# Kernel tuning notes

Hardware: AMD Instinct MI355X
Metric: run time of the kernel (lower is better)

Reference implementation:

```python
import jax, jax.numpy as jnp
import numpy as np

D = 512
EPS = 1e-5  # torch BatchNorm1d default eps


def swish(x):
    return x * jax.nn.sigmoid(x)


def batchnorm_train(x, gamma, beta):
    # BatchNorm1d in training mode: biased batch stats
    m = jnp.mean(x, axis=0)
    v = jnp.mean((x - m) ** 2, axis=0)
    return gamma * (x - m) / jnp.sqrt(v + EPS) + beta


def setup_inputs() -> dict:
    key = jax.random.key(0)
    k_fea, k_w1, k_w2, k_lerp = jax.random.split(key, 4)
    bs, P = 32768, 8192
    fea = jax.random.normal(k_fea, (bs, D), dtype=jnp.float32)
    # first P rows are the minority (positive) class
    lbl = jnp.concatenate([jnp.ones((P, 1), jnp.int32), jnp.zeros((bs - P, 1), jnp.int32)], axis=0)
    scale = 1.0 / np.sqrt(D)
    W1 = jax.random.normal(k_w1, (D, D), dtype=jnp.float32) * scale
    W2 = jax.random.normal(k_w2, (D, D), dtype=jnp.float32) * scale
    b1 = jnp.zeros((D,), jnp.float32)
    b2 = jnp.zeros((D,), jnp.float32)
    g1 = jnp.ones((D,), jnp.float32)
    g2 = jnp.ones((D,), jnp.float32)
    beta1 = jnp.zeros((D,), jnp.float32)
    beta2 = jnp.zeros((D,), jnp.float32)
    lerp_w = jax.random.uniform(k_lerp, (P, 3), dtype=jnp.float32)
    return dict(fea=fea, lbl=lbl, W1=W1, b1=b1, g1=g1, beta1=beta1,
                W2=W2, b2=b2, g2=g2, beta2=beta2, lerp_w=lerp_w, num_pos=P)


def reference(fea, lbl, W1, b1, g1, beta1, W2, b2, g2, beta2, lerp_w, num_pos):
    # fea_transform: Linear -> BN -> Swish -> Linear -> BN -> Swish
    h = swish(batchnorm_train(fea @ W1 + b1, g1, beta1))
    h = swish(batchnorm_train(h @ W2 + b2, g2, beta2))

    # SMOTE path (training mode): KNN over positive-class features
    pos_idx = jnp.nonzero(lbl[:, 0] > 0, size=num_pos)[0]  # static-size gather
    x = h[pos_idx]                                          # (P, D)
    sq = jnp.sum(x * x, axis=-1)                            # (P,)
    # negative squared pairwise distance; topk largest == nearest
    neg_dist = 2.0 * (x @ x.T) - sq[:, None] - sq[None, :]  # (P, P)
    _, idx = jax.lax.top_k(neg_dist, 3)                     # (P, 3), idx[:,0] == self

    a = x[idx[:, 0]]                                        # (P, D) anchor
    b = x[idx]                                              # (P, 3, D) neighbors
    # torch.lerp(a, b, w) = a + w * (b - a), one random w per (i, j)
    new_fea = a[:, None, :] + lerp_w[..., None] * (b - a[:, None, :])
    new_fea = new_fea.reshape(-1, D)                        # (3P, D), row-major matches i,j loop order

    fea_out = jnp.concatenate([h, new_fea], axis=0)
    lbl_out = jnp.concatenate([lbl, jnp.ones((new_fea.shape[0], 1), lbl.dtype)], axis=0)
    return fea_out, lbl_out
```

## Files before the change

kernel.cpp:

```cpp
#include <hip/hip_runtime.h>
#include <math.h>

#define NEG_INF -3.402823466e38f
#define NSPLIT 8

typedef __attribute__((ext_vector_type(8))) short bf16x8;
typedef __attribute__((ext_vector_type(4))) float f32x4;

__device__ __forceinline__ void gload_lds16(const unsigned short* g, unsigned short* l) {
  __builtin_amdgcn_global_load_lds(
      (const __attribute__((address_space(1))) unsigned int*)g,
      (__attribute__((address_space(3))) unsigned int*)l, 16, 0, 0);
}
__device__ __forceinline__ void gload_lds16f(const float* g, float* l) {
  __builtin_amdgcn_global_load_lds(
      (const __attribute__((address_space(1))) unsigned int*)g,
      (__attribute__((address_space(3))) unsigned int*)l, 16, 0, 0);
}

__device__ __forceinline__ unsigned short f2bf(float f) {
  union { float f; unsigned int u; } a; a.f = f;
  unsigned int u = a.u;
  return (unsigned short)((u + 0x7fffu + ((u >> 16) & 1u)) >> 16);
}

__device__ __forceinline__ void split3_8(f32x4 a, f32x4 b,
                                         bf16x8& hi, bf16x8& md, bf16x8& lo) {
  union { bf16x8 v; unsigned int u[4]; } H, M, L;
  float f[8];
  f[0]=a[0]; f[1]=a[1]; f[2]=a[2]; f[3]=a[3];
  f[4]=b[0]; f[5]=b[1]; f[6]=b[2]; f[7]=b[3];
#pragma unroll
  for (int p = 0; p < 4; ++p) {
    union { float f; unsigned int u; } x0, x1, h0, h1, r0, r1, m0, m1, s0, s1;
    x0.f = f[2*p]; x1.f = f[2*p+1];
    H.u[p] = (x0.u >> 16) | (x1.u & 0xffff0000u);
    h0.u = x0.u & 0xffff0000u; h1.u = x1.u & 0xffff0000u;
    r0.f = x0.f - h0.f;        r1.f = x1.f - h1.f;
    M.u[p] = (r0.u >> 16) | (r1.u & 0xffff0000u);
    m0.u = r0.u & 0xffff0000u; m1.u = r1.u & 0xffff0000u;
    s0.f = r0.f - m0.f;        s1.f = r1.f - m1.f;
    L.u[p] = (s0.u >> 16) | (s1.u & 0xffff0000u);
  }
  hi = H.v; md = M.v; lo = L.v;
}

__global__ __launch_bounds__(256) void split_w_t3(const float* __restrict__ W,
    unsigned short* __restrict__ Th, unsigned short* __restrict__ Tm,
    unsigned short* __restrict__ Tl)
{
  __shared__ float T[64][65];
  int k0 = blockIdx.x * 64, n0 = blockIdx.y * 64;
  int tid = threadIdx.x;
  int r = tid >> 4, c4 = (tid & 15) << 2;
#pragma unroll
  for (int p = 0; p < 4; ++p) {
    int row = r + p * 16;
    float4 v = *(const float4*)&W[(size_t)(k0 + row) * 512 + n0 + c4];
    T[c4 + 0][row] = v.x; T[c4 + 1][row] = v.y;
    T[c4 + 2][row] = v.z; T[c4 + 3][row] = v.w;
  }
  __syncthreads();
  int nr = tid >> 2, kc = (tid & 3) << 4;
#pragma unroll
  for (int u = 0; u < 16; ++u) {
    union { float f; unsigned int u; } x, h, rr, m, ss;
    x.f = T[nr][kc + u];
    unsigned short hb = (unsigned short)(x.u >> 16);
    h.u = x.u & 0xffff0000u;
    rr.f = x.f - h.f;
    unsigned short mb = (unsigned short)(rr.u >> 16);
    m.u = rr.u & 0xffff0000u;
    ss.f = rr.f - m.f;
    unsigned short lb = (unsigned short)(ss.u >> 16);
    size_t o = (size_t)(n0 + nr) * 512 + k0 + kc + u;
    Th[o] = hb; Tm[o] = mb; Tl[o] = lb;
  }
}

__global__ __launch_bounds__(256, 2) void gemm_split3(
    const float* __restrict__ A, const unsigned short* __restrict__ Bth,
    const unsigned short* __restrict__ Btm, const unsigned short* __restrict__ Btl,
    const float* __restrict__ bias, float* __restrict__ C, float* __restrict__ partial)
{
  __shared__ float sA[128 * 64];
  __shared__ unsigned short sBh[128 * 64];
  __shared__ unsigned short sBm[128 * 64];
  __shared__ unsigned short sBl[128 * 64];
  const int tid = threadIdx.x;
  const int w = tid >> 6, lane = tid & 63;
  const int wr = w >> 1, wc = w & 1;
  const int bm = blockIdx.x * 128, bn = blockIdx.y * 128;
  const int fr = lane & 15, fg = lane >> 4;
  const int arow = tid >> 4, acb = (tid & 15) << 4;
  const int brow = tid >> 3, bcb = (tid & 7) << 4;

  f32x4 acc[4][4];
#pragma unroll
  for (int mi = 0; mi < 4; ++mi)
#pragma unroll
    for (int ni = 0; ni < 4; ++ni) acc[mi][ni] = (f32x4){0.f, 0.f, 0.f, 0.f};

  for (int kt = 0; kt < 512; kt += 64) {
#pragma unroll
    for (int p = 0; p < 8; ++p) {
      int row = arow + p * 16;
      int swz = ((row & 3) << 5) | ((row & 4) << 2);
      int cb = acb ^ swz;
      gload_lds16f(&A[(size_t)(bm + row) * 512 + kt + (cb >> 2)],
                   &sA[row * 64 + (acb >> 2)]);
    }
#pragma unroll
    for (int p = 0; p < 4; ++p) {
      int row = brow + p * 32;
      int cb = bcb ^ ((row & 7) << 4);
      int so = (bcb >> 1);
      gload_lds16(&Bth[(size_t)(bn + row) * 512 + kt + (cb >> 1)], &sBh[row * 64 + so]);
      gload_lds16(&Btm[(size_t)(bn + row) * 512 + kt + (cb >> 1)], &sBm[row * 64 + so]);
      gload_lds16(&Btl[(size_t)(bn + row) * 512 + kt + (cb >> 1)], &sBl[row * 64 + so]);
    }
    __syncthreads();
#pragma unroll
    for (int ks = 0; ks < 2; ++ks) {
      int kbb = ks * 64 + fg * 16;
      bf16x8 bfh[4], bfm[4], bfl[4];
#pragma unroll
      for (int ni = 0; ni < 4; ++ni) {
        int row = wc * 64 + ni * 16 + fr;
        int off = row * 64 + ((kbb ^ ((row & 7) << 4)) >> 1);
        bfh[ni] = *(const bf16x8*)&sBh[off];
        bfm[ni] = *(const bf16x8*)&sBm[off];
        bfl[ni] = *(const bf16x8*)&sBl[off];
      }
      bf16x8 afh[4], afm[4], afl[4];
      int kba = ks * 128 + fg * 32;
#pragma unroll
      for (int mi = 0; mi < 4; ++mi) {
        int row = wr * 64 + mi * 16 + fr;
        int swz = ((row & 3) << 5) | ((row & 4) << 2);
        f32x4 f0 = *(const f32x4*)((const char*)sA + row * 256 + (kba ^ swz));
        f32x4 f1 = *(const f32x4*)((const char*)sA + row * 256 + ((kba + 16) ^ swz));
        split3_8(f0, f1, afh[mi], afm[mi], afl[mi]);
      }
#pragma unroll
      for (int mi = 0; mi < 4; ++mi)
#pragma unroll
        for (int ni = 0; ni < 4; ++ni) {
          acc[mi][ni] = __builtin_amdgcn_mfma_f32_16x16x32_bf16(afl[mi], bfh[ni], acc[mi][ni], 0, 0, 0);
          acc[mi][ni] = __builtin_amdgcn_mfma_f32_16x16x32_bf16(afm[mi], bfm[ni], acc[mi][ni], 0, 0, 0);
          acc[mi][ni] = __builtin_amdgcn_mfma_f32_16x16x32_bf16(afh[mi], bfl[ni], acc[mi][ni], 0, 0, 0);
          acc[mi][ni] = __builtin_amdgcn_mfma_f32_16x16x32_bf16(afm[mi], bfh[ni], acc[mi][ni], 0, 0, 0);
          acc[mi][ni] = __builtin_amdgcn_mfma_f32_16x16x32_bf16(afh[mi], bfm[ni], acc[mi][ni], 0, 0, 0);
          acc[mi][ni] = __builtin_amdgcn_mfma_f32_16x16x32_bf16(afh[mi], bfh[ni], acc[mi][ni], 0, 0, 0);
        }
    }
    __syncthreads();
  }
  float bno[4], s[4] = {0, 0, 0, 0}, q[4] = {0, 0, 0, 0};
#pragma unroll
  for (int ni = 0; ni < 4; ++ni) bno[ni] = bias[bn + wc * 64 + ni * 16 + fr];
#pragma unroll
  for (int mi = 0; mi < 4; ++mi) {
    int row = bm + wr * 64 + mi * 16 + fg * 4;
#pragma unroll
    for (int ni = 0; ni < 4; ++ni) {
      int col = bn + wc * 64 + ni * 16 + fr;
#pragma unroll
      for (int r = 0; r < 4; ++r) {
        float v = acc[mi][ni][r] + bno[ni];
        C[(size_t)(row + r) * 512 + col] = v;
        s[ni] += v; q[ni] += v * v;
      }
    }
  }
#pragma unroll
  for (int ni = 0; ni < 4; ++ni) {
    float ss = s[ni], qq = q[ni];
    ss += __shfl_xor(ss, 16); ss += __shfl_xor(ss, 32);
    qq += __shfl_xor(qq, 16); qq += __shfl_xor(qq, 32);
    if (fg == 0) {
      int slot = blockIdx.x * 2 + wr;
      int col = bn + wc * 64 + ni * 16 + fr;
      partial[(size_t)(slot * 2 + 0) * 512 + col] = ss;
      partial[(size_t)(slot * 2 + 1) * 512 + col] = qq;
    }
  }
}

__global__ __launch_bounds__(256) void bn_reduce1(
    const float* __restrict__ partial, float* __restrict__ partial2, int nslot)
{
  int g = blockIdx.x, p = blockIdx.y;
  int per = nslot >> 4;
  int t = threadIdx.x;
#pragma unroll
  for (int cc = 0; cc < 2; ++cc) {
    int c = t + cc * 256;
    float s = 0.f;
    for (int s0 = 0; s0 < per; ++s0) {
      int slot = g * per + s0;
      s += partial[(size_t)(slot * 2 + p) * 512 + c];
    }
    partial2[(size_t)(g * 2 + p) * 512 + c] = s;
  }
}

__global__ void bn_finalize(
    const float* __restrict__ partial2, const float* __restrict__ g,
    const float* __restrict__ beta, float* __restrict__ scale,
    float* __restrict__ shift, int rows)
{
  int c = blockIdx.x * blockDim.x + threadIdx.x;
  if (c >= 512) return;
  float s = 0, s2 = 0;
  for (int b = 0; b < 16; ++b) {
    s  += partial2[(size_t)(b * 2 + 0) * 512 + c];
    s2 += partial2[(size_t)(b * 2 + 1) * 512 + c];
  }
  float m = s / rows;
  float v = s2 / rows - m * m;
  if (v < 0) v = 0;
  float sc = g[c] / sqrtf(v + 1e-5f);
  scale[c] = sc;
  shift[c] = beta[c] - m * sc;
}

__global__ void bn_swish(
    const float* __restrict__ Y, const float* __restrict__ scale,
    const float* __restrict__ shift, float* __restrict__ H, int total4)
{
  int i = blockIdx.x * blockDim.x + threadIdx.x;
  if (i >= total4) return;
  float4 y = ((const float4*)Y)[i];
  int c = (i * 4) & 511;
  float z;
  float4 o;
  z = y.x * scale[c + 0] + shift[c + 0]; o.x = z / (1.f + expf(-z));
  z = y.y * scale[c + 1] + shift[c + 1]; o.y = z / (1.f + expf(-z));
  z = y.z * scale[c + 2] + shift[c + 2]; o.z = z / (1.f + expf(-z));
  z = y.w * scale[c + 3] + shift[c + 3]; o.w = z / (1.f + expf(-z));
  ((float4*)H)[i] = o;
}

__global__ void compact_pos(const int* __restrict__ lbl, int n,
                            int* __restrict__ pos, int P)
{
  __shared__ int base;
  __shared__ int wsum[16];
  int tid = threadIdx.x;
  int nthr = blockDim.x;
  for (int t = tid; t < P; t += nthr) pos[t] = 0;
  if (tid == 0) base = 0;
  __syncthreads();
  int nw = nthr >> 6;
  for (int start = 0; start < n; start += nthr) {
    int i = start + tid;
    int pred = (i < n) && (lbl[i] > 0);
    unsigned long long m = __ballot(pred);
    int wid = tid >> 6, lane = tid & 63;
    if (lane == 0) wsum[wid] = __popcll(m);
    __syncthreads();
    int wbase = 0;
    for (int w2 = 0; w2 < wid; ++w2) wbase += wsum[w2];
    int rank = base + wbase + __popcll(m & ((1ull << lane) - 1ull));
    if (pred && rank < P) pos[rank] = i;
    __syncthreads();
    if (tid == 0) { int t2 = 0; for (int w2 = 0; w2 < nw; ++w2) t2 += wsum[w2]; base += t2; }
    __syncthreads();
  }
}

__global__ void gather_sq(const float* __restrict__ H, const int* __restrict__ pos,
                          float* __restrict__ X, unsigned short* __restrict__ Xh,
                          float* __restrict__ sq)
{
  int r = blockIdx.x, t = threadIdx.x;
  int src = pos[r];
  float4 v = *(const float4*)&H[src * 512 + t * 4];
  *(float4*)&X[r * 512 + t * 4] = v;
  ushort4 hv;
  hv.x = f2bf(v.x); hv.y = f2bf(v.y); hv.z = f2bf(v.z); hv.w = f2bf(v.w);
  *(ushort4*)&Xh[r * 512 + t * 4] = hv;
  float s = v.x * v.x + v.y * v.y + v.z * v.z + v.w * v.w;
#pragma unroll
  for (int off = 32; off > 0; off >>= 1) s += __shfl_down(s, off);
  __shared__ float red[2];
  if ((t & 63) == 0) red[t >> 6] = s;
  __syncthreads();
  if (t == 0) sq[r] = red[0] + red[1];
}

__global__ __launch_bounds__(256, 2) void gram8(
    const unsigned short* __restrict__ Xh, const float* __restrict__ sq, int P,
    float* __restrict__ p8v, int* __restrict__ p8j)
{
  __shared__ unsigned short Ah[128 * 64];
  __shared__ unsigned short Bh[128 * 64];
  __shared__ float dl[4][64][17];
  __shared__ float sqj_l[128];

  const int tid = threadIdx.x;
  const int w = tid >> 6, lane = tid & 63;
  const int wr = w >> 1, wc = w & 1;
  const int bi = blockIdx.x * 128;
  const int jchunk = P / NSPLIT;
  const int jlo = blockIdx.y * jchunk;

  const int srow = tid >> 3;
  const int scb  = (tid & 7) << 4;
  const int fr = lane & 15, fg = lane >> 4;

  float t[8]; int ji[8];
#pragma unroll
  for (int q = 0; q < 8; ++q) { t[q] = NEG_INF; ji[q] = 0x7fffffff; }

  for (int jt = 0; jt < jchunk; jt += 128) {
    const int j0 = jlo + jt;
    if (tid < 128) sqj_l[tid] = sq[j0 + tid];
    f32x4 acc[4][4];
#pragma unroll
    for (int mi = 0; mi < 4; ++mi)
#pragma unroll
      for (int ni = 0; ni < 4; ++ni) acc[mi][ni] = (f32x4){0.f, 0.f, 0.f, 0.f};

    for (int kt = 0; kt < 512; kt += 64) {
#pragma unroll
      for (int it = 0; it < 4; ++it) {
        int row = srow + it * 32;
        int cb = scb ^ ((row & 7) << 4);
        gload_lds16(&Xh[(size_t)(bi + row) * 512 + kt + (cb >> 1)],
                    &Ah[row * 64 + (scb >> 1)]);
        gload_lds16(&Xh[(size_t)(j0 + row) * 512 + kt + (cb >> 1)],
                    &Bh[row * 64 + (scb >> 1)]);
      }
      __syncthreads();
#pragma unroll
      for (int ks = 0; ks < 2; ++ks) {
        bf16x8 af[4], bfr[4];
        int kb = ks * 64 + fg * 16;
#pragma unroll
        for (int mi = 0; mi < 4; ++mi) {
          int row = wr * 64 + mi * 16 + fr;
          af[mi] = *(const bf16x8*)&Ah[row * 64 + ((kb ^ ((row & 7) << 4)) >> 1)];
        }
#pragma unroll
        for (int ni = 0; ni < 4; ++ni) {
          int row = wc * 64 + ni * 16 + fr;
          bfr[ni] = *(const bf16x8*)&Bh[row * 64 + ((kb ^ ((row & 7) << 4)) >> 1)];
        }
#pragma unroll
        for (int mi = 0; mi < 4; ++mi)
#pragma unroll
          for (int ni = 0; ni < 4; ++ni)
            acc[mi][ni] = __builtin_amdgcn_mfma_f32_16x16x32_bf16(
                af[mi], bfr[ni], acc[mi][ni], 0, 0, 0);
      }
      __syncthreads();
    }

#pragma unroll
    for (int qn = 0; qn < 4; ++qn) {
      float sqv = sqj_l[wc * 64 + qn * 16 + fr];
#pragma unroll
      for (int mi = 0; mi < 4; ++mi)
#pragma unroll
        for (int r = 0; r < 4; ++r)
          dl[w][mi * 16 + fg * 4 + r][fr] = 2.0f * acc[mi][qn][r] - sqv;
      __syncthreads();
      int jbase = j0 + wc * 64 + qn * 16;
      for (int c = 0; c < 16; ++c) {
        float v = dl[w][lane][c];
        if (v > t[7]) {
          t[7] = v; ji[7] = jbase + c;
#pragma unroll
          for (int q = 7; q > 0; --q) {
            if (t[q] > t[q - 1]) {
              float tv = t[q]; t[q] = t[q - 1]; t[q - 1] = tv;
              int tj = ji[q]; ji[q] = ji[q - 1]; ji[q - 1] = tj;
            }
          }
        }
      }
      __syncthreads();
    }
  }

  int row = bi + wr * 64 + lane;
  int set = blockIdx.y * 2 + wc;
  size_t base = ((size_t)row * (NSPLIT * 2) + set) * 8;
#pragma unroll
  for (int q = 0; q < 8; ++q) { p8v[base + q] = t[q]; p8j[base + q] = ji[q]; }
}

__global__ void merge8(const float* __restrict__ p8v, const int* __restrict__ p8j,
                       int* __restrict__ cand, int P)
{
  int i = blockIdx.x * blockDim.x + threadIdx.x;
  if (i >= P) return;
  const int S = NSPLIT * 2;
  int head[S];
#pragma unroll
  for (int s = 0; s < S; ++s) head[s] = 0;
  const float* v = p8v + (size_t)i * S * 8;
  const int* j = p8j + (size_t)i * S * 8;
  for (int k = 0; k < 8; ++k) {
    float bv = NEG_INF; int bj = 0x7fffffff; int bs = 0;
#pragma unroll
    for (int s = 0; s < S; ++s) {
      if (head[s] < 8) {
        float vv = v[s * 8 + head[s]];
        int jj = j[s * 8 + head[s]];
        if (vv > bv || (vv == bv && jj < bj)) { bv = vv; bj = jj; bs = s; }
      }
    }
    head[bs]++;
    cand[i * 8 + k] = bj;
  }
}

__global__ __launch_bounds__(64) void rescore(
    const float* __restrict__ X, const float* __restrict__ sq,
    const int* __restrict__ cand, int* __restrict__ idx3)
{
  int i = blockIdx.x;
  int lane = threadIdx.x;
  f32x4 x0 = *(const f32x4*)&X[(size_t)i * 512 + lane * 8];
  f32x4 x1 = *(const f32x4*)&X[(size_t)i * 512 + lane * 8 + 4];
  float d[8]; int cj[8];
#pragma unroll
  for (int c = 0; c < 8; ++c) {
    int j = cand[i * 8 + c];
    cj[c] = j;
    f32x4 y0 = *(const f32x4*)&X[(size_t)j * 512 + lane * 8];
    f32x4 y1 = *(const f32x4*)&X[(size_t)j * 512 + lane * 8 + 4];
    float p = x0.x * y0.x + x0.y * y0.y + x0.z * y0.z + x0.w * y0.w
            + x1.x * y1.x + x1.y * y1.y + x1.z * y1.z + x1.w * y1.w;
#pragma unroll
    for (int off = 32; off > 0; off >>= 1) p += __shfl_xor(p, off);
    d[c] = 2.0f * p - sq[i] - sq[j];
  }
  if (lane == 0) {
    for (int k = 0; k < 3; ++k) {
      int b = 0;
#pragma unroll
      for (int c = 1; c < 8; ++c)
        if (d[c] > d[b] || (d[c] == d[b] && cj[c] < cj[b])) b = c;
      idx3[i * 3 + k] = cj[b];
      d[b] = NEG_INF; cj[b] = 0x7fffffff;
    }
  }
}

__global__ void make_newfea(const float* __restrict__ X, const int* __restrict__ idx3,
                            const float* __restrict__ lw, float* __restrict__ out)
{
  int r = blockIdx.x;
  int i = r / 3, k = r - i * 3;
  int ai = idx3[i * 3 + 0];
  int bi = idx3[i * 3 + k];
  float w = lw[r];
  int t = threadIdx.x;
  float4 av = *(const float4*)&X[ai * 512 + t * 4];
  float4 bv = *(const float4*)&X[bi * 512 + t * 4];
  float4 o;
  o.x = av.x + w * (bv.x - av.x);
  o.y = av.y + w * (bv.y - av.y);
  o.z = av.z + w * (bv.z - av.z);
  o.w = av.w + w * (bv.w - av.w);
  *(float4*)&out[(size_t)r * 512 + t * 4] = o;
}

__global__ void write_lbl(const int* __restrict__ lbl, float* __restrict__ out,
                          int n_in, int n_total)
{
  int i = blockIdx.x * blockDim.x + threadIdx.x;
  if (i < n_total) out[i] = (i < n_in) ? (float)lbl[i] : 1.0f;
}

extern "C" void kernel_launch(void* const* d_in, const int* in_sizes, int n_in,
                              void* d_out, int out_size, void* d_ws, size_t ws_size,
                              hipStream_t stream)
{
  const float* fea   = (const float*)d_in[0];
  const int*   lbl   = (const int*)d_in[1];
  const float* W1    = (const float*)d_in[2];
  const float* b1    = (const float*)d_in[3];
  const float* g1    = (const float*)d_in[4];
  const float* beta1 = (const float*)d_in[5];
  const float* W2    = (const float*)d_in[6];
  const float* b2    = (const float*)d_in[7];
  const float* g2    = (const float*)d_in[8];
  const float* beta2 = (const float*)d_in[9];
  const float* lerp_w = (const float*)d_in[10];

  int bs = in_sizes[0] / 512;
  int P  = in_sizes[10] / 3;
  int n_total = bs + 3 * P;

  float* out_f = (float*)d_out;
  float* Hout = out_f;
  float* newfea = out_f + (size_t)bs * 512;
  float* lbl_out = out_f + (size_t)n_total * 512;

  const size_t MB = 1024 * 1024;
  const size_t KB = 1024;
  char* ws = (char*)d_ws;
  float* Y1 = (float*)ws;
  float* X  = (float*)(ws + 64 * MB);
  unsigned short* W1h = (unsigned short*)(ws + 64 * MB);
  unsigned short* W1m = (unsigned short*)(ws + 64 * MB + 512 * KB);
  unsigned short* W1l = (unsigned short*)(ws + 64 * MB + 1024 * KB);
  unsigned short* W2h = (unsigned short*)(ws + 64 * MB + 1536 * KB);
  unsigned short* W2m = (unsigned short*)(ws + 64 * MB + 2048 * KB);
  unsigned short* W2l = (unsigned short*)(ws + 64 * MB + 2560 * KB);
  float* partial = (float*)(ws + 80 * MB);
  float* scale = (float*)(ws + 82 * MB);
  float* shiftv = scale + 512;
  float* sq = shiftv + 512;
  int* pos = (int*)(sq + 8192);
  int* idx3 = pos + 8192;
  float* partial2 = (float*)(ws + 83 * MB);
  unsigned short* Xh = (unsigned short*)ws;
  float* p8v = (float*)(ws + 8 * MB);
  int*   p8j = (int*)(ws + 12 * MB);
  int*   cand = (int*)(ws + 16 * MB);

  dim3 wgrid(8, 8);
  split_w_t3<<<wgrid, 256, 0, stream>>>(W1, W1h, W1m, W1l);
  split_w_t3<<<wgrid, 256, 0, stream>>>(W2, W2h, W2m, W2l);

  dim3 ggrid(bs / 128, 4);
  int nslot = (bs / 128) * 2;
  dim3 rgrid(16, 2);

  gemm_split3<<<ggrid, 256, 0, stream>>>(fea, W1h, W1m, W1l, b1, Y1, partial);
  bn_reduce1<<<rgrid, 256, 0, stream>>>(partial, partial2, nslot);
  bn_finalize<<<2, 256, 0, stream>>>(partial2, g1, beta1, scale, shiftv, bs);
  bn_swish<<<(bs * 512 / 4 + 255) / 256, 256, 0, stream>>>(Y1, scale, shiftv, Y1, bs * 512 / 4);

  gemm_split3<<<ggrid, 256, 0, stream>>>(Y1, W2h, W2m, W2l, b2, Hout, partial);
  bn_reduce1<<<rgrid, 256, 0, stream>>>(partial, partial2, nslot);
  bn_finalize<<<2, 256, 0, stream>>>(partial2, g2, beta2, scale, shiftv, bs);
  bn_swish<<<(bs * 512 / 4 + 255) / 256, 256, 0, stream>>>(Hout, scale, shiftv, Hout, bs * 512 / 4);

  compact_pos<<<1, 1024, 0, stream>>>(lbl, bs, pos, P);
  gather_sq<<<P, 128, 0, stream>>>(Hout, pos, X, Xh, sq);

  dim3 gram_grid(P / 128, NSPLIT);
  gram8<<<gram_grid, 256, 0, stream>>>(Xh, sq, P, p8v, p8j);
  merge8<<<(P + 255) / 256, 256, 0, stream>>>(p8v, p8j, cand, P);
  rescore<<<P, 64, 0, stream>>>(X, sq, cand, idx3);

  make_newfea<<<3 * P, 128, 0, stream>>>(X, idx3, lerp_w, newfea);
  write_lbl<<<(n_total + 255) / 256, 256, 0, stream>>>(lbl, lbl_out, bs, n_total);
}
```

Baseline: 541.2 us.

## Double-buffer GEMM and Gram loads, keep top-k in registers, parallelize compaction

The split-bf16 GEMM now uses double-buffered LDS stages with a K-step of 32, so the next tile's global-to-LDS load overlaps the current MFMA work. The Gram/top-k kernel is flattened into one double-buffered stream over (j-tile, k-tile) stages. Each lane keeps per-row top-8 lists in registers straight from the accumulators, replacing the LDS transpose and its extra barriers, then merges four partial lists at the end. The single-block label compaction becomes a three-kernel count/prefix/scatter. This adds two launches and more register pressure in the Gram kernel.

```diff
diff --git a/kernel.cpp b/kernel.cpp
--- a/kernel.cpp
+++ b/kernel.cpp
@@ -83,17 +83,14 @@
     const unsigned short* __restrict__ Btm, const unsigned short* __restrict__ Btl,
     const float* __restrict__ bias, float* __restrict__ C, float* __restrict__ partial)
 {
-  __shared__ float sA[128 * 64];
-  __shared__ unsigned short sBh[128 * 64];
-  __shared__ unsigned short sBm[128 * 64];
-  __shared__ unsigned short sBl[128 * 64];
+  __shared__ char smem[81920];
   const int tid = threadIdx.x;
   const int w = tid >> 6, lane = tid & 63;
   const int wr = w >> 1, wc = w & 1;
   const int bm = blockIdx.x * 128, bn = blockIdx.y * 128;
   const int fr = lane & 15, fg = lane >> 4;
-  const int arow = tid >> 4, acb = (tid & 15) << 4;
-  const int brow = tid >> 3, bcb = (tid & 7) << 4;
+  const int arow = tid >> 3, acb = (tid & 7) << 4;
+  const int brow = tid >> 2, bcb = (tid & 3) << 4;
 
   f32x4 acc[4][4];
 #pragma unroll
@@ -101,59 +98,68 @@
 #pragma unroll
     for (int ni = 0; ni < 4; ++ni) acc[mi][ni] = (f32x4){0.f, 0.f, 0.f, 0.f};
 
-  for (int kt = 0; kt < 512; kt += 64) {
-#pragma unroll
-    for (int p = 0; p < 8; ++p) {
-      int row = arow + p * 16;
-      int swz = ((row & 3) << 5) | ((row & 4) << 2);
-      int cb = acb ^ swz;
-      gload_lds16f(&A[(size_t)(bm + row) * 512 + kt + (cb >> 2)],
-                   &sA[row * 64 + (acb >> 2)]);
-    }
+  auto STAGE = [&](int buf, int ktf) {
+    float* sA = (float*)(smem + buf * 40960);
+    unsigned short* sBh = (unsigned short*)(smem + buf * 40960 + 16384);
+    unsigned short* sBm = sBh + 4096;
+    unsigned short* sBl = sBm + 4096;
 #pragma unroll
     for (int p = 0; p < 4; ++p) {
-      int row = brow + p * 32;
-      int cb = bcb ^ ((row & 7) << 4);
-      int so = (bcb >> 1);
-      gload_lds16(&Bth[(size_t)(bn + row) * 512 + kt + (cb >> 1)], &sBh[row * 64 + so]);
-      gload_lds16(&Btm[(size_t)(bn + row) * 512 + kt + (cb >> 1)], &sBm[row * 64 + so]);
-      gload_lds16(&Btl[(size_t)(bn + row) * 512 + kt + (cb >> 1)], &sBl[row * 64 + so]);
-    }
-    __syncthreads();
-#pragma unroll
-    for (int ks = 0; ks < 2; ++ks) {
-      int kbb = ks * 64 + fg * 16;
-      bf16x8 bfh[4], bfm[4], bfl[4];
+      int row = arow + p * 32;
+      int cb = acb ^ ((row & 7) << 4);
+      gload_lds16f(&A[(size_t)(bm + row) * 512 + ktf + (cb >> 2)],
+                   &sA[row * 32 + (acb >> 2)]);
+    }
+#pragma unroll
+    for (int p = 0; p < 2; ++p) {
+      int row = brow + p * 64;
+      int cb = bcb ^ (((row >> 1) & 3) << 4);
+      int so = row * 32 + (bcb >> 1);
+      gload_lds16(&Bth[(size_t)(bn + row) * 512 + ktf + (cb >> 1)], &sBh[so]);
+      gload_lds16(&Btm[(size_t)(bn + row) * 512 + ktf + (cb >> 1)], &sBm[so]);
+      gload_lds16(&Btl[(size_t)(bn + row) * 512 + ktf + (cb >> 1)], &sBl[so]);
+    }
+  };
+
+  STAGE(0, 0);
+  __syncthreads();
+  for (int it = 0; it < 16; ++it) {
+    int cur = it & 1;
+    if (it + 1 < 16) STAGE(cur ^ 1, (it + 1) * 32);
+    float* sA = (float*)(smem + cur * 40960);
+    unsigned short* sBh = (unsigned short*)(smem + cur * 40960 + 16384);
+    unsigned short* sBm = sBh + 4096;
+    unsigned short* sBl = sBm + 4096;
+    bf16x8 bh[4], bmf[4], blf[4];
+#pragma unroll
+    for (int ni = 0; ni < 4; ++ni) {
+      int row = wc * 64 + ni * 16 + fr;
+      int off = row * 32 + (((fg * 16) ^ (((row >> 1) & 3) << 4)) >> 1);
+      bh[ni]  = *(const bf16x8*)&sBh[off];
+      bmf[ni] = *(const bf16x8*)&sBm[off];
+      blf[ni] = *(const bf16x8*)&sBl[off];
+    }
+    bf16x8 ah[4], am[4], al[4];
+#pragma unroll
+    for (int mi = 0; mi < 4; ++mi) {
+      int row = wr * 64 + mi * 16 + fr;
+      int swz = (row & 7) << 4;
+      const char* rb = (const char*)(sA + row * 32);
+      f32x4 f0 = *(const f32x4*)(rb + ((fg * 32) ^ swz));
+      f32x4 f1 = *(const f32x4*)(rb + ((fg * 32 + 16) ^ swz));
+      split3_8(f0, f1, ah[mi], am[mi], al[mi]);
+    }
+#pragma unroll
+    for (int mi = 0; mi < 4; ++mi)
 #pragma unroll
       for (int ni = 0; ni < 4; ++ni) {
-        int row = wc * 64 + ni * 16 + fr;
-        int off = row * 64 + ((kbb ^ ((row & 7) << 4)) >> 1);
-        bfh[ni] = *(const bf16x8*)&sBh[off];
-        bfm[ni] = *(const bf16x8*)&sBm[off];
-        bfl[ni] = *(const bf16x8*)&sBl[off];
+        acc[mi][ni] = __builtin_amdgcn_mfma_f32_16x16x32_bf16(al[mi], bh[ni],  acc[mi][ni], 0, 0, 0);
+        acc[mi][ni] = __builtin_amdgcn_mfma_f32_16x16x32_bf16(am[mi], bmf[ni], acc[mi][ni], 0, 0, 0);
+        acc[mi][ni] = __builtin_amdgcn_mfma_f32_16x16x32_bf16(ah[mi], blf[ni], acc[mi][ni], 0, 0, 0);
+        acc[mi][ni] = __builtin_amdgcn_mfma_f32_16x16x32_bf16(am[mi], bh[ni],  acc[mi][ni], 0, 0, 0);
+        acc[mi][ni] = __builtin_amdgcn_mfma_f32_16x16x32_bf16(ah[mi], bmf[ni], acc[mi][ni], 0, 0, 0);
+        acc[mi][ni] = __builtin_amdgcn_mfma_f32_16x16x32_bf16(ah[mi], bh[ni],  acc[mi][ni], 0, 0, 0);
       }
-      bf16x8 afh[4], afm[4], afl[4];
-      int kba = ks * 128 + fg * 32;
-#pragma unroll
-      for (int mi = 0; mi < 4; ++mi) {
-        int row = wr * 64 + mi * 16 + fr;
-        int swz = ((row & 3) << 5) | ((row & 4) << 2);
-        f32x4 f0 = *(const f32x4*)((const char*)sA + row * 256 + (kba ^ swz));
-        f32x4 f1 = *(const f32x4*)((const char*)sA + row * 256 + ((kba + 16) ^ swz));
-        split3_8(f0, f1, afh[mi], afm[mi], afl[mi]);
-      }
-#pragma unroll
-      for (int mi = 0; mi < 4; ++mi)
-#pragma unroll
-        for (int ni = 0; ni < 4; ++ni) {
-          acc[mi][ni] = __builtin_amdgcn_mfma_f32_16x16x32_bf16(afl[mi], bfh[ni], acc[mi][ni], 0, 0, 0);
-          acc[mi][ni] = __builtin_amdgcn_mfma_f32_16x16x32_bf16(afm[mi], bfm[ni], acc[mi][ni], 0, 0, 0);
-          acc[mi][ni] = __builtin_amdgcn_mfma_f32_16x16x32_bf16(afh[mi], bfl[ni], acc[mi][ni], 0, 0, 0);
-          acc[mi][ni] = __builtin_amdgcn_mfma_f32_16x16x32_bf16(afm[mi], bfh[ni], acc[mi][ni], 0, 0, 0);
-          acc[mi][ni] = __builtin_amdgcn_mfma_f32_16x16x32_bf16(afh[mi], bfm[ni], acc[mi][ni], 0, 0, 0);
-          acc[mi][ni] = __builtin_amdgcn_mfma_f32_16x16x32_bf16(afh[mi], bfh[ni], acc[mi][ni], 0, 0, 0);
-        }
-    }
     __syncthreads();
   }
   float bno[4], s[4] = {0, 0, 0, 0}, q[4] = {0, 0, 0, 0};
@@ -242,32 +248,45 @@
   ((float4*)H)[i] = o;
 }
 
-__global__ void compact_pos(const int* __restrict__ lbl, int n,
-                            int* __restrict__ pos, int P)
-{
-  __shared__ int base;
-  __shared__ int wsum[16];
-  int tid = threadIdx.x;
-  int nthr = blockDim.x;
-  for (int t = tid; t < P; t += nthr) pos[t] = 0;
-  if (tid == 0) base = 0;
+__global__ __launch_bounds__(1024) void pos_count(const int* __restrict__ lbl, int n,
+                                                  int* __restrict__ cnt,
+                                                  int* __restrict__ pos, int P)
+{
+  int b = blockIdx.x, tid = threadIdx.x;
+  int i = b * 1024 + tid;
+  if (i < P) pos[i] = 0;
+  int pred = (i < n) && (lbl[i] > 0);
+  unsigned long long m = __ballot(pred);
+  __shared__ int ws[16];
+  if ((tid & 63) == 0) ws[tid >> 6] = __popcll(m);
   __syncthreads();
-  int nw = nthr >> 6;
-  for (int start = 0; start < n; start += nthr) {
-    int i = start + tid;
-    int pred = (i < n) && (lbl[i] > 0);
-    unsigned long long m = __ballot(pred);
-    int wid = tid >> 6, lane = tid & 63;
-    if (lane == 0) wsum[wid] = __popcll(m);
-    __syncthreads();
-    int wbase = 0;
-    for (int w2 = 0; w2 < wid; ++w2) wbase += wsum[w2];
-    int rank = base + wbase + __popcll(m & ((1ull << lane) - 1ull));
-    if (pred && rank < P) pos[rank] = i;
-    __syncthreads();
-    if (tid == 0) { int t2 = 0; for (int w2 = 0; w2 < nw; ++w2) t2 += wsum[w2]; base += t2; }
-    __syncthreads();
-  }
+  if (tid == 0) { int s = 0; for (int k = 0; k < 16; ++k) s += ws[k]; cnt[b] = s; }
+}
+
+__global__ void pos_prefix(int* __restrict__ cnt, int nb)
+{
+  if (threadIdx.x == 0) {
+    int s = 0;
+    for (int b = 0; b < nb; ++b) { int c = cnt[b]; cnt[b] = s; s += c; }
+  }
+}
+
+__global__ __launch_bounds__(1024) void pos_scatter(const int* __restrict__ lbl, int n,
+                                                    const int* __restrict__ cntp,
+                                                    int* __restrict__ pos, int P)
+{
+  int b = blockIdx.x, tid = threadIdx.x;
+  int i = b * 1024 + tid;
+  int pred = (i < n) && (lbl[i] > 0);
+  unsigned long long m = __ballot(pred);
+  __shared__ int ws[16];
+  int wid = tid >> 6, lane = tid & 63;
+  if (lane == 0) ws[wid] = __popcll(m);
+  __syncthreads();
+  int wbase = 0;
+  for (int w2 = 0; w2 < wid; ++w2) wbase += ws[w2];
+  int rank = cntp[b] + wbase + __popcll(m & ((1ull << lane) - 1ull));
+  if (pred && rank < P) pos[rank] = i;
 }
 
 __global__ void gather_sq(const float* __restrict__ H, const int* __restrict__ pos,
@@ -294,102 +313,140 @@
     const unsigned short* __restrict__ Xh, const float* __restrict__ sq, int P,
     float* __restrict__ p8v, int* __restrict__ p8j)
 {
-  __shared__ unsigned short Ah[128 * 64];
-  __shared__ unsigned short Bh[128 * 64];
-  __shared__ float dl[4][64][17];
-  __shared__ float sqj_l[128];
+  __shared__ char smem[65536];
+  __shared__ float sqj_l[2][128];
 
   const int tid = threadIdx.x;
   const int w = tid >> 6, lane = tid & 63;
-  const int wr = w >> 1, wc = w & 1;
+  const int ih = w >> 1, jh = w & 1;
   const int bi = blockIdx.x * 128;
   const int jchunk = P / NSPLIT;
   const int jlo = blockIdx.y * jchunk;
+  const int ntile = jchunk >> 7;
+  const int total = ntile * 8;
 
   const int srow = tid >> 3;
-  const int scb  = (tid & 7) << 4;
+  const int scb = (tid & 7) << 4;
   const int fr = lane & 15, fg = lane >> 4;
 
-  float t[8]; int ji[8];
-#pragma unroll
-  for (int q = 0; q < 8; ++q) { t[q] = NEG_INF; ji[q] = 0x7fffffff; }
-
-  for (int jt = 0; jt < jchunk; jt += 128) {
-    const int j0 = jlo + jt;
-    if (tid < 128) sqj_l[tid] = sq[j0 + tid];
-    f32x4 acc[4][4];
-#pragma unroll
-    for (int mi = 0; mi < 4; ++mi)
-#pragma unroll
-      for (int ni = 0; ni < 4; ++ni) acc[mi][ni] = (f32x4){0.f, 0.f, 0.f, 0.f};
-
-    for (int kt = 0; kt < 512; kt += 64) {
-#pragma unroll
-      for (int it = 0; it < 4; ++it) {
-        int row = srow + it * 32;
-        int cb = scb ^ ((row & 7) << 4);
-        gload_lds16(&Xh[(size_t)(bi + row) * 512 + kt + (cb >> 1)],
-                    &Ah[row * 64 + (scb >> 1)]);
-        gload_lds16(&Xh[(size_t)(j0 + row) * 512 + kt + (cb >> 1)],
-                    &Bh[row * 64 + (scb >> 1)]);
+  float t8[4][8]; int j8[4][8];
+#pragma unroll
+  for (int mi = 0; mi < 4; ++mi)
+#pragma unroll
+    for (int q = 0; q < 8; ++q) { t8[mi][q] = NEG_INF; j8[mi][q] = 0x7fffffff; }
+
+  auto STAGE = [&](int s) {
+    int kt = (s & 7) << 6;
+    int j0 = jlo + ((s >> 3) << 7);
+    unsigned short* bA = (unsigned short*)(smem + ((s & 1) << 15));
+    unsigned short* bB = bA + 8192;
+#pragma unroll
+    for (int it = 0; it < 4; ++it) {
+      int row = srow + it * 32;
+      int cb = scb ^ ((row & 7) << 4);
+      gload_lds16(&Xh[(size_t)(bi + row) * 512 + kt + (cb >> 1)], &bA[row * 64 + (scb >> 1)]);
+      gload_lds16(&Xh[(size_t)(j0 + row) * 512 + kt + (cb >> 1)], &bB[row * 64 + (scb >> 1)]);
+    }
+  };
+
+  STAGE(0);
+  if (tid < 128) sqj_l[0][tid] = sq[jlo + tid];
+  __syncthreads();
+
+  f32x4 acc[4][4];
+  for (int s = 0; s < total; ++s) {
+    if ((s & 7) == 0) {
+#pragma unroll
+      for (int a = 0; a < 4; ++a)
+#pragma unroll
+        for (int b = 0; b < 4; ++b) acc[a][b] = (f32x4){0.f, 0.f, 0.f, 0.f};
+    }
+    if (s + 1 < total) {
+      STAGE(s + 1);
+      if (((s + 1) & 7) == 0) {
+        int jt1 = (s + 1) >> 3;
+        if (tid < 128) sqj_l[jt1 & 1][tid] = sq[jlo + (jt1 << 7) + tid];
       }
-      __syncthreads();
-#pragma unroll
-      for (int ks = 0; ks < 2; ++ks) {
-        bf16x8 af[4], bfr[4];
-        int kb = ks * 64 + fg * 16;
+    }
+    unsigned short* bA = (unsigned short*)(smem + ((s & 1) << 15));
+    unsigned short* bB = bA + 8192;
+#pragma unroll
+    for (int ks = 0; ks < 2; ++ks) {
+      bf16x8 af[4], bfr[4];
+      int kb = ks * 64 + fg * 16;
+#pragma unroll
+      for (int mi = 0; mi < 4; ++mi) {
+        int row = ih * 64 + mi * 16 + fr;
+        af[mi] = *(const bf16x8*)&bA[row * 64 + ((kb ^ ((row & 7) << 4)) >> 1)];
+      }
+#pragma unroll
+      for (int nj = 0; nj < 4; ++nj) {
+        int row = jh * 64 + nj * 16 + fr;
+        bfr[nj] = *(const bf16x8*)&bB[row * 64 + ((kb ^ ((row & 7) << 4)) >> 1)];
+      }
+#pragma unroll
+      for (int nj = 0; nj < 4; ++nj)
+#pragma unroll
+        for (int mi = 0; mi < 4; ++mi)
+          acc[nj][mi] = __builtin_amdgcn_mfma_f32_16x16x32_bf16(
+              bfr[nj], af[mi], acc[nj][mi], 0, 0, 0);
+    }
+    if ((s & 7) == 7) {
+      int jt = s >> 3;
+      int j0 = jlo + (jt << 7);
+      int par = jt & 1;
+#pragma unroll
+      for (int nj = 0; nj < 4; ++nj) {
+        f32x4 sv = *(const f32x4*)&sqj_l[par][jh * 64 + nj * 16 + fg * 4];
+        int jb = j0 + jh * 64 + nj * 16 + fg * 4;
 #pragma unroll
         for (int mi = 0; mi < 4; ++mi) {
-          int row = wr * 64 + mi * 16 + fr;
-          af[mi] = *(const bf16x8*)&Ah[row * 64 + ((kb ^ ((row & 7) << 4)) >> 1)];
-        }
-#pragma unroll
-        for (int ni = 0; ni < 4; ++ni) {
-          int row = wc * 64 + ni * 16 + fr;
-          bfr[ni] = *(const bf16x8*)&Bh[row * 64 + ((kb ^ ((row & 7) << 4)) >> 1)];
-        }
-#pragma unroll
-        for (int mi = 0; mi < 4; ++mi)
-#pragma unroll
-          for (int ni = 0; ni < 4; ++ni)
-            acc[mi][ni] = __builtin_amdgcn_mfma_f32_16x16x32_bf16(
-                af[mi], bfr[ni], acc[mi][ni], 0, 0, 0);
-      }
-      __syncthreads();
-    }
-
-#pragma unroll
-    for (int qn = 0; qn < 4; ++qn) {
-      float sqv = sqj_l[wc * 64 + qn * 16 + fr];
-#pragma unroll
-      for (int mi = 0; mi < 4; ++mi)
-#pragma unroll
-        for (int r = 0; r < 4; ++r)
-          dl[w][mi * 16 + fg * 4 + r][fr] = 2.0f * acc[mi][qn][r] - sqv;
-      __syncthreads();
-      int jbase = j0 + wc * 64 + qn * 16;
-      for (int c = 0; c < 16; ++c) {
-        float v = dl[w][lane][c];
-        if (v > t[7]) {
-          t[7] = v; ji[7] = jbase + c;
-#pragma unroll
-          for (int q = 7; q > 0; --q) {
-            if (t[q] > t[q - 1]) {
-              float tv = t[q]; t[q] = t[q - 1]; t[q - 1] = tv;
-              int tj = ji[q]; ji[q] = ji[q - 1]; ji[q - 1] = tj;
+#pragma unroll
+          for (int r = 0; r < 4; ++r) {
+            float v = 2.0f * acc[nj][mi][r] - sv[r];
+            if (v > t8[mi][7]) {
+              t8[mi][7] = v; j8[mi][7] = jb + r;
+#pragma unroll
+              for (int q = 7; q > 0; --q)
+                if (t8[mi][q] > t8[mi][q - 1]) {
+                  float tv = t8[mi][q]; t8[mi][q] = t8[mi][q - 1]; t8[mi][q - 1] = tv;
+                  int tj = j8[mi][q]; j8[mi][q] = j8[mi][q - 1]; j8[mi][q - 1] = tj;
+                }
             }
           }
         }
       }
-      __syncthreads();
-    }
-  }
-
-  int row = bi + wr * 64 + lane;
-  int set = blockIdx.y * 2 + wc;
-  size_t base = ((size_t)row * (NSPLIT * 2) + set) * 8;
-#pragma unroll
-  for (int q = 0; q < 8; ++q) { p8v[base + q] = t[q]; p8j[base + q] = ji[q]; }
+    }
+    __syncthreads();
+  }
+
+  float* mv = (float*)smem;
+  int* mj = (int*)(smem + 32768);
+#pragma unroll
+  for (int mi = 0; mi < 4; ++mi)
+#pragma unroll
+    for (int q = 0; q < 8; ++q) {
+      int idx = ((w * 4 + mi) * 16 + fr) * 32 + fg * 8 + q;
+      mv[idx] = t8[mi][q]; mj[idx] = j8[mi][q];
+    }
+  __syncthreads();
+  {
+    int mi = lane >> 4, cc = lane & 15;
+    int base = ((w * 4 + mi) * 16 + cc) * 32;
+    int h0 = 0, h1 = 0, h2 = 0, h3 = 0;
+    int i = bi + ih * 64 + mi * 16 + cc;
+    int set = blockIdx.y * 2 + jh;
+    size_t ob = ((size_t)i * (NSPLIT * 2) + set) * 8;
+    for (int k = 0; k < 8; ++k) {
+      float bv = NEG_INF; int bj = 0x7fffffff; int bg = 0;
+      { float v = mv[base + h0];      int jj = mj[base + h0];      if (h0 < 8 && (v > bv || (v == bv && jj < bj))) { bv = v; bj = jj; bg = 0; } }
+      { float v = mv[base + 8 + h1];  int jj = mj[base + 8 + h1];  if (h1 < 8 && (v > bv || (v == bv && jj < bj))) { bv = v; bj = jj; bg = 1; } }
+      { float v = mv[base + 16 + h2]; int jj = mj[base + 16 + h2]; if (h2 < 8 && (v > bv || (v == bv && jj < bj))) { bv = v; bj = jj; bg = 2; } }
+      { float v = mv[base + 24 + h3]; int jj = mj[base + 24 + h3]; if (h3 < 8 && (v > bv || (v == bv && jj < bj))) { bv = v; bj = jj; bg = 3; } }
+      h0 += (bg == 0); h1 += (bg == 1); h2 += (bg == 2); h3 += (bg == 3);
+      p8v[ob + k] = bv; p8j[ob + k] = bj;
+    }
+  }
 }
 
 __global__ void merge8(const float* __restrict__ p8v, const int* __restrict__ p8j,
@@ -519,6 +576,7 @@
   float* sq = shiftv + 512;
   int* pos = (int*)(sq + 8192);
   int* idx3 = pos + 8192;
+  int* cnt = idx3 + 3 * 8192;
   float* partial2 = (float*)(ws + 83 * MB);
   unsigned short* Xh = (unsigned short*)ws;
   float* p8v = (float*)(ws + 8 * MB);
@@ -543,7 +601,10 @@
   bn_finalize<<<2, 256, 0, stream>>>(partial2, g2, beta2, scale, shiftv, bs);
   bn_swish<<<(bs * 512 / 4 + 255) / 256, 256, 0, stream>>>(Hout, scale, shiftv, Hout, bs * 512 / 4);
 
-  compact_pos<<<1, 1024, 0, stream>>>(lbl, bs, pos, P);
+  int nb = (bs + 1023) / 1024;
+  pos_count<<<nb, 1024, 0, stream>>>(lbl, bs, cnt, pos, P);
+  pos_prefix<<<1, 64, 0, stream>>>(cnt, nb);
+  pos_scatter<<<nb, 1024, 0, stream>>>(lbl, bs, cnt, pos, P);
   gather_sq<<<P, 128, 0, stream>>>(Hout, pos, X, Xh, sq);
 
   dim3 gram_grid(P / 128, NSPLIT);
```

Measured after the change: 536.5 us. No clear change (-0.9%).
